# Optimization experiments

Hardware: AMD Instinct MI355X
Metric: run time of the kernel (lower is better)

Reference implementation:

```python
import jax, jax.numpy as jnp
import numpy as np

N_NODES = 100000
N_EDGES = 1600000
IN, HID, OUT = 512, 128, 64


def setup_inputs() -> dict:
    key = jax.random.key(0)
    ks = jax.random.split(key, 7)
    x = jax.random.normal(ks[0], (N_NODES, IN), dtype=jnp.float32)
    rows = jax.random.randint(ks[1], (N_EDGES,), 0, N_NODES, dtype=jnp.int32)
    cols = jax.random.randint(ks[2], (N_EDGES,), 0, N_NODES, dtype=jnp.int32)
    vals = jax.random.uniform(ks[3], (N_EDGES,), dtype=jnp.float32)
    # torch.nn.Linear weights have shape (out_features, in_features)
    W0 = jax.random.normal(ks[4], (HID, IN), dtype=jnp.float32) * (IN ** -0.5)
    W1 = jax.random.normal(ks[5], (HID, HID), dtype=jnp.float32) * (HID ** -0.5)
    W2 = jax.random.normal(ks[6], (OUT, HID), dtype=jnp.float32) * (HID ** -0.5)
    return {"x": x, "rows": rows, "cols": cols, "vals": vals,
            "W0": W0, "W1": W1, "W2": W2}


def reference(x, rows, cols, vals, W0, W1, W2):
    n = x.shape[0]

    def spmm(h):  # out[r] = sum_e vals[e] * h[cols[e]] for rows[e] == r
        return jax.ops.segment_sum(vals[:, None] * h[cols], rows, num_segments=n)

    # layer 0: Linear -> SpMM -> ReLU (dropout p=0.0 is identity)
    h = jax.nn.relu(spmm(x @ W0.T))
    # layer 1
    h = jax.nn.relu(spmm(h @ W1.T))
    # output layer: Linear -> SpMM (no activation)
    return spmm(h @ W2.T)
```

## Files before the change

kernel.cpp:

```cpp
#include <hip/hip_runtime.h>
#include <hip/hip_bf16.h>
#include <cstddef>


typedef unsigned short ushort_t;
using frag_t = __attribute__((ext_vector_type(8))) short;
using accf4 = __attribute__((ext_vector_type(4))) float;

__device__ __forceinline__ ushort_t f2bf(float f) {
    unsigned int u = __float_as_uint(f);
    u += 0x7FFF + ((u >> 16) & 1);
    return (ushort_t)(u >> 16);
}
__device__ __forceinline__ float bf2f(unsigned int u16) {
    return __uint_as_float(u16 << 16);
}


__device__ void gemm0_body(int bx, const float* __restrict__ A,
                           const float* __restrict__ W, ushort_t* __restrict__ C,
                           int M) {
    constexpr int K = 512, N = 128, BM = 128, BN = 128, BK = 64;
    constexpr int WM = BM / 2, WN = BN / 2;
    constexpr int TI = WM / 16, TJ = WN / 16;
    constexpr int LDA = BK + 8;
    constexpr int T = K / BK;
    constexpr int A_PER = BM * BK / 4 / 256;
    constexpr int B_PER = BN * BK / 4 / 256;

    __shared__ __align__(16) ushort_t As[BM][LDA];
    __shared__ __align__(16) ushort_t Bs[BN][LDA];

    const int tid = threadIdx.x;
    const int lane = tid & 63;
    const int wid = tid >> 6;
    const int wm = wid >> 1, wn = wid & 1;
    const int rowBase = bx * BM;
    const int lrow = lane & 15, kq = lane >> 4;

    float4 aF[A_PER], bF[B_PER];

    auto loadTile = [&](int k0) {
#pragma unroll
        for (int i = 0; i < A_PER; i++) {
            int idx = tid + i * 256;
            int r = idx / (BK / 4), c4 = idx % (BK / 4);
            int grow = rowBase + r;
            aF[i] = (grow < M) ? *(const float4*)(A + (size_t)grow * K + k0 + c4 * 4)
                               : make_float4(0.f, 0.f, 0.f, 0.f);
        }
#pragma unroll
        for (int i = 0; i < B_PER; i++) {
            int idx = tid + i * 256;
            int r = idx / (BK / 4), c4 = idx % (BK / 4);
            bF[i] = *(const float4*)(W + (size_t)r * K + k0 + c4 * 4);
        }
    };
    auto storeTile = [&]() {
#pragma unroll
        for (int i = 0; i < A_PER; i++) {
            int idx = tid + i * 256;
            int r = idx / (BK / 4), c4 = idx % (BK / 4);
            ushort_t p[4] = {f2bf(aF[i].x), f2bf(aF[i].y), f2bf(aF[i].z), f2bf(aF[i].w)};
            *(uint2*)&As[r][c4 * 4] = *(uint2*)p;
        }
#pragma unroll
        for (int i = 0; i < B_PER; i++) {
            int idx = tid + i * 256;
            int r = idx / (BK / 4), c4 = idx % (BK / 4);
            ushort_t p[4] = {f2bf(bF[i].x), f2bf(bF[i].y), f2bf(bF[i].z), f2bf(bF[i].w)};
            *(uint2*)&Bs[r][c4 * 4] = *(uint2*)p;
        }
    };

    accf4 acc[TI][TJ];
#pragma unroll
    for (int i = 0; i < TI; i++)
#pragma unroll
        for (int j = 0; j < TJ; j++) acc[i][j] = accf4{0.f, 0.f, 0.f, 0.f};

    loadTile(0);
    storeTile();
    __syncthreads();

    for (int t = 0; t < T; t++) {
        if (t + 1 < T) loadTile((t + 1) * BK);
#pragma unroll
        for (int ks = 0; ks < BK / 32; ks++) {
            const int kb = ks * 32 + kq * 8;
            frag_t a[TI], b[TJ];
#pragma unroll
            for (int i = 0; i < TI; i++)
                a[i] = *(const frag_t*)&As[wm * WM + i * 16 + lrow][kb];
#pragma unroll
            for (int j = 0; j < TJ; j++)
                b[j] = *(const frag_t*)&Bs[wn * WN + j * 16 + lrow][kb];
#pragma unroll
            for (int i = 0; i < TI; i++)
#pragma unroll
                for (int j = 0; j < TJ; j++)
                    acc[i][j] = __builtin_amdgcn_mfma_f32_16x16x32_bf16(
                        a[i], b[j], acc[i][j], 0, 0, 0);
        }
        __syncthreads();
        if (t + 1 < T) {
            storeTile();
            __syncthreads();
        }
    }

#pragma unroll
    for (int i = 0; i < TI; i++) {
#pragma unroll
        for (int j = 0; j < TJ; j++) {
            int col = wn * WN + j * 16 + lrow;
#pragma unroll
            for (int r = 0; r < 4; r++) {
                int grow = rowBase + wm * WM + i * 16 + kq * 4 + r;
                if (grow < M) C[(size_t)grow * N + col] = f2bf(acc[i][j][r]);
            }
        }
    }
}

__global__ __launch_bounds__(256) void d1_k(const float* __restrict__ x,
                                            const float* __restrict__ W0,
                                            ushort_t* __restrict__ g0, int M,
                                            int* __restrict__ cnt8, int m8,
                                            const float* __restrict__ W1,
                                            const float* __restrict__ W2,
                                            ushort_t* __restrict__ Wb1,
                                            ushort_t* __restrict__ Wb2,
                                            int gblocks) {
    if ((int)blockIdx.x < gblocks) {
        gemm0_body(blockIdx.x, x, W0, g0, M);
    } else {
        int i = ((int)blockIdx.x - gblocks) * 256 + threadIdx.x;
        if (i < m8) cnt8[i] = 0;
        if (i < 16384) Wb1[i] = f2bf(W1[i]);
        else if (i < 24576) Wb2[i - 16384] = f2bf(W2[i - 16384]);
    }
}


__global__ __launch_bounds__(256) void block_totals(const int* __restrict__ counts,
                                                    int* __restrict__ bsums, int n) {
    __shared__ int s[256];
    int t = threadIdx.x;
    int i = blockIdx.x * 256 + t;
    s[t] = (i < n) ? counts[i] : 0;
    __syncthreads();
    for (int off = 128; off > 0; off >>= 1) {
        if (t < off) s[t] += s[t + off];
        __syncthreads();
    }
    if (t == 0) bsums[blockIdx.x] = s[0];
}

__global__ __launch_bounds__(256) void block_totals_t(const int* __restrict__ cnt8,
                                                      int* __restrict__ bsums,
                                                      int n, int m8) {
    __shared__ int s[256];
    int t = threadIdx.x;
    int i = blockIdx.x * 256 + t;
    s[t] = (i < m8) ? cnt8[(i & 7) * n + (i >> 3)] : 0;
    __syncthreads();
    for (int off = 128; off > 0; off >>= 1) {
        if (t < off) s[t] += s[t + off];
        __syncthreads();
    }
    if (t == 0) bsums[blockIdx.x] = s[0];
}

__global__ __launch_bounds__(512) void scan_sums(int* bsums, int nb) {
    __shared__ int s[512];
    int t = threadIdx.x;
    int v = (t < nb) ? bsums[t] : 0;
    s[t] = v;
    __syncthreads();
    for (int off = 1; off < 512; off *= 2) {
        int u = (t >= off) ? s[t - off] : 0;
        __syncthreads();
        s[t] += u;
        __syncthreads();
    }
    if (t < nb) bsums[t] = s[t] - v;
}

__global__ __launch_bounds__(256) void scan_wo(const int* __restrict__ data,
                                               const int* __restrict__ offs,
                                               int* __restrict__ out0, int m) {
    __shared__ int s[256];
    int t = threadIdx.x;
    int i = blockIdx.x * 256 + t;
    int v = (i < m) ? data[i] : 0;
    s[t] = v;
    __syncthreads();
    for (int off = 1; off < 256; off *= 2) {
        int u = (t >= off) ? s[t - off] : 0;
        __syncthreads();
        s[t] += u;
        __syncthreads();
    }
    if (i < m) out0[i] = s[t] - v + offs[blockIdx.x];
}

__global__ __launch_bounds__(256) void scan_final(const int* __restrict__ cnt8,
                                                  const int* __restrict__ offs,
                                                  int* __restrict__ dstbase,
                                                  int* __restrict__ row_ptr,
                                                  int n, int ne, int m8) {
    __shared__ int s[256];
    int t = threadIdx.x;
    int i = blockIdx.x * 256 + t;
    int v = (i < m8) ? cnt8[(i & 7) * n + (i >> 3)] : 0;
    s[t] = v;
    __syncthreads();
    for (int off = 1; off < 256; off *= 2) {
        int u = (t >= off) ? s[t - off] : 0;
        __syncthreads();
        s[t] += u;
        __syncthreads();
    }
    int excl = s[t] - v + offs[blockIdx.x];
    if (i < m8) {
        dstbase[i] = excl;
        if ((i & 7) == 0) row_ptr[i >> 3] = excl;
    }
    if (i == 0) row_ptr[n] = ne;
}


__global__ __launch_bounds__(256) void hist8_k(const int* __restrict__ rows,
                                               int* __restrict__ cnt8,
                                               int* __restrict__ rank,
                                               int n, int ne) {
    int e = blockIdx.x * 256 + threadIdx.x;
    if (e >= ne) return;
    int s = blockIdx.x & 7;
    rank[e] = atomicAdd(&cnt8[s * n + rows[e]], 1);
}

__global__ __launch_bounds__(256) void scatter8_k(const int* __restrict__ rows,
                                                  const int* __restrict__ cols,
                                                  const float* __restrict__ vals,
                                                  const int* __restrict__ dstbase,
                                                  const int* __restrict__ rank,
                                                  int2* __restrict__ es, int ne) {
    int e = blockIdx.x * 256 + threadIdx.x;
    if (e >= ne) return;
    int s = blockIdx.x & 7;
    int r = rows[e];
    int p = dstbase[r * 8 + s] + rank[e];
    es[p] = make_int2(cols[e], __float_as_int(vals[e]));
}


__device__ __forceinline__ void acc8(float* acc, uint4 q, float v) {
    acc[0] += v * bf2f(q.x & 0xffff); acc[1] += v * bf2f(q.x >> 16);
    acc[2] += v * bf2f(q.y & 0xffff); acc[3] += v * bf2f(q.y >> 16);
    acc[4] += v * bf2f(q.z & 0xffff); acc[5] += v * bf2f(q.z >> 16);
    acc[6] += v * bf2f(q.w & 0xffff); acc[7] += v * bf2f(q.w >> 16);
}
__device__ __forceinline__ void acc4f(float* acc, uint2 q, float v) {
    acc[0] += v * bf2f(q.x & 0xffff); acc[1] += v * bf2f(q.x >> 16);
    acc[2] += v * bf2f(q.y & 0xffff); acc[3] += v * bf2f(q.y >> 16);
}

template <int NOUT>
__global__ __launch_bounds__(256) void spmm_mfma(const int* __restrict__ row_ptr,
                                                 const int2* __restrict__ es,
                                                 const ushort_t* __restrict__ G,
                                                 const ushort_t* __restrict__ Wb,
                                                 ushort_t* __restrict__ Hout, int n) {
    constexpr int TJ = NOUT / 64;
    constexpr int SEG = NOUT / 8;

    __shared__ __align__(16) ushort_t Hs[16][136];
    __shared__ __align__(16) ushort_t Os[16][NOUT + 8];

    const int tid = threadIdx.x;
    const int lane = tid & 63;
    const int wid = tid >> 6;
    const int g = lane >> 4, lg = lane & 15;
    const int lrow = lane & 15, kq = lane >> 4;
    const int rowBase = blockIdx.x * 16;

    frag_t bfr[4][TJ];
#pragma unroll
    for (int ks = 0; ks < 4; ks++)
#pragma unroll
        for (int j = 0; j < TJ; j++)
            bfr[ks][j] = *(const frag_t*)&Wb[(size_t)(wid * 16 * TJ + j * 16 + lrow) * 128 +
                                             ks * 32 + kq * 8];

    const ushort_t* __restrict__ Gp = G + lg * 8;
#pragma unroll
    for (int q = 0; q < 4; q++) {
        int row = rowBase + wid * 4 + q;
        float acc[8];
#pragma unroll
        for (int k = 0; k < 8; k++) acc[k] = 0.f;
        if (row < n) {
            int s = row_ptr[row];
            int e = row_ptr[row + 1];
            for (int p = s; p < e; p += 16) {
#pragma unroll
                for (int u = 0; u < 4; u++) {
                    int idx = p + u * 4 + g;
                    if (idx < e) {
                        int2 ed = es[idx];
                        uint4 qv = *(const uint4*)(Gp + (size_t)ed.x * 128);
                        acc8(acc, qv, __int_as_float(ed.y));
                    }
                }
            }
        }
#pragma unroll
        for (int k = 0; k < 8; k++) {
            acc[k] += __shfl_xor(acc[k], 16);
            acc[k] += __shfl_xor(acc[k], 32);
        }
        if (g == 0) {
            uint4 o;
            float a0 = fmaxf(acc[0], 0.f), a1 = fmaxf(acc[1], 0.f);
            float a2 = fmaxf(acc[2], 0.f), a3 = fmaxf(acc[3], 0.f);
            float a4 = fmaxf(acc[4], 0.f), a5 = fmaxf(acc[5], 0.f);
            float a6 = fmaxf(acc[6], 0.f), a7 = fmaxf(acc[7], 0.f);
            o.x = (unsigned)f2bf(a0) | ((unsigned)f2bf(a1) << 16);
            o.y = (unsigned)f2bf(a2) | ((unsigned)f2bf(a3) << 16);
            o.z = (unsigned)f2bf(a4) | ((unsigned)f2bf(a5) << 16);
            o.w = (unsigned)f2bf(a6) | ((unsigned)f2bf(a7) << 16);
            *(uint4*)&Hs[wid * 4 + q][lg * 8] = o;
        }
    }
    __syncthreads();

    accf4 oacc[TJ];
#pragma unroll
    for (int j = 0; j < TJ; j++) oacc[j] = accf4{0.f, 0.f, 0.f, 0.f};
#pragma unroll
    for (int ks = 0; ks < 4; ks++) {
        frag_t a = *(const frag_t*)&Hs[lrow][ks * 32 + kq * 8];
#pragma unroll
        for (int j = 0; j < TJ; j++)
            oacc[j] = __builtin_amdgcn_mfma_f32_16x16x32_bf16(a, bfr[ks][j], oacc[j], 0, 0, 0);
    }
#pragma unroll
    for (int j = 0; j < TJ; j++) {
        int col = wid * 16 * TJ + j * 16 + lrow;
#pragma unroll
        for (int r = 0; r < 4; r++) Os[kq * 4 + r][col] = f2bf(oacc[j][r]);
    }
    __syncthreads();

    if (tid < 16 * SEG) {
        int row16 = tid / SEG, sg = tid % SEG;
        if (rowBase + row16 < n)
            *(uint4*)&Hout[(size_t)(rowBase + row16) * NOUT + sg * 8] =
                *(const uint4*)&Os[row16][sg * 8];
    }
}


__global__ __launch_bounds__(256) void spmm_csr_64f(const int* __restrict__ row_ptr,
                                                    const int2* __restrict__ es,
                                                    const ushort_t* __restrict__ G,
                                                    float* __restrict__ H, int n) {
    int row = blockIdx.x * 4 + (threadIdx.x >> 6);
    int lane = threadIdx.x & 63;
    int g = lane >> 4, lg = lane & 15;
    if (row >= n) return;
    int s = row_ptr[row];
    int e = row_ptr[row + 1];
    float acc[4] = {0.f, 0.f, 0.f, 0.f};
    const ushort_t* __restrict__ Gp = G + lg * 4;
    for (int p = s; p < e; p += 16) {
#pragma unroll
        for (int u = 0; u < 4; u++) {
            int idx = p + u * 4 + g;
            if (idx < e) {
                int2 e0 = es[idx];
                uint2 q0 = *(const uint2*)(Gp + (size_t)e0.x * 64);
                acc4f(acc, q0, __int_as_float(e0.y));
            }
        }
    }
#pragma unroll
    for (int k = 0; k < 4; k++) {
        acc[k] += __shfl_xor(acc[k], 16);
        acc[k] += __shfl_xor(acc[k], 32);
    }
    if (g == 0) {
        float4 o = make_float4(acc[0], acc[1], acc[2], acc[3]);
        *(float4*)(H + (size_t)row * 64 + lg * 4) = o;
    }
}

static inline size_t align_up(size_t x, size_t a) { return (x + a - 1) & ~(a - 1); }

extern "C" void kernel_launch(void* const* d_in, const int* in_sizes, int n_in,
                              void* d_out, int out_size, void* d_ws, size_t ws_size,
                              hipStream_t stream) {
    const float* x = (const float*)d_in[0];
    const int* rows = (const int*)d_in[1];
    const int* cols = (const int*)d_in[2];
    const float* vals = (const float*)d_in[3];
    const float* W0 = (const float*)d_in[4];
    const float* W1 = (const float*)d_in[5];
    const float* W2 = (const float*)d_in[6];
    float* out = (float*)d_out;

    const int IN = 512, HID = 128, OUT = 64;
    const int n = in_sizes[0] / IN;
    const int ne = in_sizes[1];
    (void)OUT;

    char* ws = (char*)d_ws;
    size_t off = 0;
    ushort_t* g0 = (ushort_t*)(ws + off); off = align_up(off + (size_t)n * HID * 2, 512);
    ushort_t* g1 = (ushort_t*)(ws + off); off = align_up(off + (size_t)n * HID * 2, 512);
    ushort_t* g2 = (ushort_t*)(ws + off); off = align_up(off + (size_t)n * 64 * 2, 512);
    int2* es2 = (int2*)(ws + off); off = align_up(off + (size_t)ne * 8, 512);
    int* cnt8 = (int*)(ws + off); off = align_up(off + (size_t)8 * n * 4, 512);
    int* rank = (int*)(ws + off); off = align_up(off + (size_t)ne * 4, 512);
    int* dstbase = (int*)(ws + off); off = align_up(off + (size_t)8 * n * 4, 512);
    int* row_ptr = (int*)(ws + off); off = align_up(off + (size_t)(n + 1) * 4, 512);
    int* bsum0 = (int*)(ws + off); off = align_up(off + 4096 * 4, 512);
    int* bsum1 = (int*)(ws + off); off = align_up(off + 512 * 4, 512);
    int* off0 = (int*)(ws + off); off = align_up(off + 4096 * 4, 512);
    ushort_t* Wb1 = (ushort_t*)(ws + off); off = align_up(off + (size_t)HID * HID * 2, 512);
    ushort_t* Wb2 = (ushort_t*)(ws + off); off = align_up(off + (size_t)64 * HID * 2, 512);

    const int eb = (ne + 255) / 256;
    const int m8 = 8 * n;
    const int nb8 = (m8 + 255) / 256;
    const int nb8b = (nb8 + 255) / 256;
    const int gblocks = (n + 127) / 128;
    const int fblocks = (n + 15) / 16;
    const int sblocks = (n + 3) / 4;

    d1_k<<<gblocks + nb8, 256, 0, stream>>>(x, W0, g0, n, cnt8, m8, W1, W2,
                                            Wb1, Wb2, gblocks);

    hist8_k<<<eb, 256, 0, stream>>>(rows, cnt8, rank, n, ne);
    block_totals_t<<<nb8, 256, 0, stream>>>(cnt8, bsum0, n, m8);
    block_totals<<<nb8b, 256, 0, stream>>>(bsum0, bsum1, nb8);
    scan_sums<<<1, 512, 0, stream>>>(bsum1, nb8b);
    scan_wo<<<nb8b, 256, 0, stream>>>(bsum0, bsum1, off0, nb8);
    scan_final<<<nb8, 256, 0, stream>>>(cnt8, off0, dstbase, row_ptr, n, ne, m8);
    scatter8_k<<<eb, 256, 0, stream>>>(rows, cols, vals, dstbase, rank, es2, ne);

    spmm_mfma<128><<<fblocks, 256, 0, stream>>>(row_ptr, es2, g0, Wb1, g1, n);
    spmm_mfma<64><<<fblocks, 256, 0, stream>>>(row_ptr, es2, g1, Wb2, g2, n);
    spmm_csr_64f<<<sblocks, 256, 0, stream>>>(row_ptr, es2, g2, out, n);
}
```

Baseline: 666.7 us.

## Interleave two-row gathers in SpMM and collapse multi-level scan into one kernel

The SpMM gather loops now handle two rows per wavefront at once. Each iteration batch-loads the edges of both rows, then issues all feature-row loads before any accumulation, which raises memory-level parallelism for the random gathers. Padding edges are skipped by testing whether the value is zero. The three-kernel middle level of the prefix scan becomes a single 1024-thread kernel scanning four elements per thread, removing two launches. The pairing can waste lanes when the two rows differ in degree, and explicit edges with value 0.0 are also skipped, which is harmless because they contribute nothing.

```diff
diff --git a/kernel.cpp b/kernel.cpp
--- a/kernel.cpp
+++ b/kernel.cpp
@@ -143,20 +143,6 @@
 }
 
 
-__global__ __launch_bounds__(256) void block_totals(const int* __restrict__ counts,
-                                                    int* __restrict__ bsums, int n) {
-    __shared__ int s[256];
-    int t = threadIdx.x;
-    int i = blockIdx.x * 256 + t;
-    s[t] = (i < n) ? counts[i] : 0;
-    __syncthreads();
-    for (int off = 128; off > 0; off >>= 1) {
-        if (t < off) s[t] += s[t + off];
-        __syncthreads();
-    }
-    if (t == 0) bsums[blockIdx.x] = s[0];
-}
-
 __global__ __launch_bounds__(256) void block_totals_t(const int* __restrict__ cnt8,
                                                       int* __restrict__ bsums,
                                                       int n, int m8) {
@@ -172,37 +158,28 @@
     if (t == 0) bsums[blockIdx.x] = s[0];
 }
 
-__global__ __launch_bounds__(512) void scan_sums(int* bsums, int nb) {
-    __shared__ int s[512];
+__global__ __launch_bounds__(1024) void scan_mid(int* bsums, int nb) {
+    __shared__ int s[1024];
     int t = threadIdx.x;
-    int v = (t < nb) ? bsums[t] : 0;
-    s[t] = v;
-    __syncthreads();
-    for (int off = 1; off < 512; off *= 2) {
+    int base = t * 4;
+    int v0 = (base + 0 < nb) ? bsums[base + 0] : 0;
+    int v1 = (base + 1 < nb) ? bsums[base + 1] : 0;
+    int v2 = (base + 2 < nb) ? bsums[base + 2] : 0;
+    int v3 = (base + 3 < nb) ? bsums[base + 3] : 0;
+    int l0 = v0, l1 = l0 + v1, l2 = l1 + v2, l3 = l2 + v3;
+    s[t] = l3;
+    __syncthreads();
+    for (int off = 1; off < 1024; off *= 2) {
         int u = (t >= off) ? s[t - off] : 0;
         __syncthreads();
         s[t] += u;
         __syncthreads();
     }
-    if (t < nb) bsums[t] = s[t] - v;
-}
-
-__global__ __launch_bounds__(256) void scan_wo(const int* __restrict__ data,
-                                               const int* __restrict__ offs,
-                                               int* __restrict__ out0, int m) {
-    __shared__ int s[256];
-    int t = threadIdx.x;
-    int i = blockIdx.x * 256 + t;
-    int v = (i < m) ? data[i] : 0;
-    s[t] = v;
-    __syncthreads();
-    for (int off = 1; off < 256; off *= 2) {
-        int u = (t >= off) ? s[t - off] : 0;
-        __syncthreads();
-        s[t] += u;
-        __syncthreads();
-    }
-    if (i < m) out0[i] = s[t] - v + offs[blockIdx.x];
+    int excl = s[t] - l3;
+    if (base + 0 < nb) bsums[base + 0] = excl;
+    if (base + 1 < nb) bsums[base + 1] = excl + l0;
+    if (base + 2 < nb) bsums[base + 2] = excl + l1;
+    if (base + 3 < nb) bsums[base + 3] = excl + l2;
 }
 
 __global__ __launch_bounds__(256) void scan_final(const int* __restrict__ cnt8,
@@ -267,6 +244,46 @@
     acc[2] += v * bf2f(q.y & 0xffff); acc[3] += v * bf2f(q.y >> 16);
 }
 
+__device__ __forceinline__ void gather_pair_128(const int* __restrict__ row_ptr,
+                                                const int2* __restrict__ es,
+                                                const ushort_t* __restrict__ Gp,
+                                                int rowA, int rowB, int n,
+                                                int g, float* accA, float* accB) {
+    int sA = 0, eA = 0, sB = 0, eB = 0;
+    if (rowA < n) { sA = row_ptr[rowA]; eA = row_ptr[rowA + 1]; }
+    if (rowB < n) { sB = row_ptr[rowB]; eB = row_ptr[rowB + 1]; }
+    int nbA = (eA - sA + 15) >> 4, nbB = (eB - sB + 15) >> 4;
+    int nb = nbA > nbB ? nbA : nbB;
+    for (int b = 0; b < nb; b++) {
+        int2 edA[4], edB[4];
+#pragma unroll
+        for (int u = 0; u < 4; u++) {
+            int ia = sA + b * 16 + u * 4 + g;
+            edA[u] = (ia < eA) ? es[ia] : make_int2(0, 0);
+        }
+#pragma unroll
+        for (int u = 0; u < 4; u++) {
+            int ib = sB + b * 16 + u * 4 + g;
+            edB[u] = (ib < eB) ? es[ib] : make_int2(0, 0);
+        }
+        uint4 qA[4], qB[4];
+#pragma unroll
+        for (int u = 0; u < 4; u++) {
+            qA[u] = make_uint4(0, 0, 0, 0);
+            if (edA[u].y) qA[u] = *(const uint4*)(Gp + (size_t)edA[u].x * 128);
+        }
+#pragma unroll
+        for (int u = 0; u < 4; u++) {
+            qB[u] = make_uint4(0, 0, 0, 0);
+            if (edB[u].y) qB[u] = *(const uint4*)(Gp + (size_t)edB[u].x * 128);
+        }
+#pragma unroll
+        for (int u = 0; u < 4; u++) acc8(accA, qA[u], __int_as_float(edA[u].y));
+#pragma unroll
+        for (int u = 0; u < 4; u++) acc8(accB, qB[u], __int_as_float(edB[u].y));
+    }
+}
+
 template <int NOUT>
 __global__ __launch_bounds__(256) void spmm_mfma(const int* __restrict__ row_ptr,
                                                  const int2* __restrict__ es,
@@ -286,6 +303,40 @@
     const int lrow = lane & 15, kq = lane >> 4;
     const int rowBase = blockIdx.x * 16;
 
+    const ushort_t* __restrict__ Gp = G + lg * 8;
+#pragma unroll
+    for (int pr = 0; pr < 2; pr++) {
+        int rowA = rowBase + wid * 4 + pr * 2;
+        int rowB = rowA + 1;
+        float accA[8], accB[8];
+#pragma unroll
+        for (int k = 0; k < 8; k++) { accA[k] = 0.f; accB[k] = 0.f; }
+        gather_pair_128(row_ptr, es, Gp, rowA, rowB, n, g, accA, accB);
+#pragma unroll
+        for (int k = 0; k < 8; k++) {
+            accA[k] += __shfl_xor(accA[k], 16);
+            accA[k] += __shfl_xor(accA[k], 32);
+            accB[k] += __shfl_xor(accB[k], 16);
+            accB[k] += __shfl_xor(accB[k], 32);
+        }
+        if (g == 0) {
+            uint4 o;
+            o.x = (unsigned)f2bf(fmaxf(accA[0], 0.f)) | ((unsigned)f2bf(fmaxf(accA[1], 0.f)) << 16);
+            o.y = (unsigned)f2bf(fmaxf(accA[2], 0.f)) | ((unsigned)f2bf(fmaxf(accA[3], 0.f)) << 16);
+            o.z = (unsigned)f2bf(fmaxf(accA[4], 0.f)) | ((unsigned)f2bf(fmaxf(accA[5], 0.f)) << 16);
+            o.w = (unsigned)f2bf(fmaxf(accA[6], 0.f)) | ((unsigned)f2bf(fmaxf(accA[7], 0.f)) << 16);
+            *(uint4*)&Hs[wid * 4 + pr * 2][lg * 8] = o;
+        }
+        if (g == 1) {
+            uint4 o;
+            o.x = (unsigned)f2bf(fmaxf(accB[0], 0.f)) | ((unsigned)f2bf(fmaxf(accB[1], 0.f)) << 16);
+            o.y = (unsigned)f2bf(fmaxf(accB[2], 0.f)) | ((unsigned)f2bf(fmaxf(accB[3], 0.f)) << 16);
+            o.z = (unsigned)f2bf(fmaxf(accB[4], 0.f)) | ((unsigned)f2bf(fmaxf(accB[5], 0.f)) << 16);
+            o.w = (unsigned)f2bf(fmaxf(accB[6], 0.f)) | ((unsigned)f2bf(fmaxf(accB[7], 0.f)) << 16);
+            *(uint4*)&Hs[wid * 4 + pr * 2 + 1][lg * 8] = o;
+        }
+    }
+
     frag_t bfr[4][TJ];
 #pragma unroll
     for (int ks = 0; ks < 4; ks++)
@@ -293,47 +344,6 @@
         for (int j = 0; j < TJ; j++)
             bfr[ks][j] = *(const frag_t*)&Wb[(size_t)(wid * 16 * TJ + j * 16 + lrow) * 128 +
                                              ks * 32 + kq * 8];
-
-    const ushort_t* __restrict__ Gp = G + lg * 8;
-#pragma unroll
-    for (int q = 0; q < 4; q++) {
-        int row = rowBase + wid * 4 + q;
-        float acc[8];
-#pragma unroll
-        for (int k = 0; k < 8; k++) acc[k] = 0.f;
-        if (row < n) {
-            int s = row_ptr[row];
-            int e = row_ptr[row + 1];
-            for (int p = s; p < e; p += 16) {
-#pragma unroll
-                for (int u = 0; u < 4; u++) {
-                    int idx = p + u * 4 + g;
-                    if (idx < e) {
-                        int2 ed = es[idx];
-                        uint4 qv = *(const uint4*)(Gp + (size_t)ed.x * 128);
-                        acc8(acc, qv, __int_as_float(ed.y));
-                    }
-                }
-            }
-        }
-#pragma unroll
-        for (int k = 0; k < 8; k++) {
-            acc[k] += __shfl_xor(acc[k], 16);
-            acc[k] += __shfl_xor(acc[k], 32);
-        }
-        if (g == 0) {
-            uint4 o;
-            float a0 = fmaxf(acc[0], 0.f), a1 = fmaxf(acc[1], 0.f);
-            float a2 = fmaxf(acc[2], 0.f), a3 = fmaxf(acc[3], 0.f);
-            float a4 = fmaxf(acc[4], 0.f), a5 = fmaxf(acc[5], 0.f);
-            float a6 = fmaxf(acc[6], 0.f), a7 = fmaxf(acc[7], 0.f);
-            o.x = (unsigned)f2bf(a0) | ((unsigned)f2bf(a1) << 16);
-            o.y = (unsigned)f2bf(a2) | ((unsigned)f2bf(a3) << 16);
-            o.z = (unsigned)f2bf(a4) | ((unsigned)f2bf(a5) << 16);
-            o.w = (unsigned)f2bf(a6) | ((unsigned)f2bf(a7) << 16);
-            *(uint4*)&Hs[wid * 4 + q][lg * 8] = o;
-        }
-    }
     __syncthreads();
 
     accf4 oacc[TJ];
@@ -367,33 +377,62 @@
                                                     const int2* __restrict__ es,
                                                     const ushort_t* __restrict__ G,
                                                     float* __restrict__ H, int n) {
-    int row = blockIdx.x * 4 + (threadIdx.x >> 6);
-    int lane = threadIdx.x & 63;
-    int g = lane >> 4, lg = lane & 15;
-    if (row >= n) return;
-    int s = row_ptr[row];
-    int e = row_ptr[row + 1];
-    float acc[4] = {0.f, 0.f, 0.f, 0.f};
+    const int lane = threadIdx.x & 63;
+    const int wid = threadIdx.x >> 6;
+    const int g = lane >> 4, lg = lane & 15;
+    const int rowA = blockIdx.x * 8 + wid * 2;
+    const int rowB = rowA + 1;
+
+    int sA = 0, eA = 0, sB = 0, eB = 0;
+    if (rowA < n) { sA = row_ptr[rowA]; eA = row_ptr[rowA + 1]; }
+    if (rowB < n) { sB = row_ptr[rowB]; eB = row_ptr[rowB + 1]; }
+    int nbA = (eA - sA + 15) >> 4, nbB = (eB - sB + 15) >> 4;
+    int nb = nbA > nbB ? nbA : nbB;
+
+    float accA[4] = {0.f, 0.f, 0.f, 0.f}, accB[4] = {0.f, 0.f, 0.f, 0.f};
     const ushort_t* __restrict__ Gp = G + lg * 4;
-    for (int p = s; p < e; p += 16) {
-#pragma unroll
-        for (int u = 0; u < 4; u++) {
-            int idx = p + u * 4 + g;
-            if (idx < e) {
-                int2 e0 = es[idx];
-                uint2 q0 = *(const uint2*)(Gp + (size_t)e0.x * 64);
-                acc4f(acc, q0, __int_as_float(e0.y));
-            }
-        }
+    for (int b = 0; b < nb; b++) {
+        int2 edA[4], edB[4];
+#pragma unroll
+        for (int u = 0; u < 4; u++) {
+            int ia = sA + b * 16 + u * 4 + g;
+            edA[u] = (ia < eA) ? es[ia] : make_int2(0, 0);
+        }
+#pragma unroll
+        for (int u = 0; u < 4; u++) {
+            int ib = sB + b * 16 + u * 4 + g;
+            edB[u] = (ib < eB) ? es[ib] : make_int2(0, 0);
+        }
+        uint2 qA[4], qB[4];
+#pragma unroll
+        for (int u = 0; u < 4; u++) {
+            qA[u] = make_uint2(0, 0);
+            if (edA[u].y) qA[u] = *(const uint2*)(Gp + (size_t)edA[u].x * 64);
+        }
+#pragma unroll
+        for (int u = 0; u < 4; u++) {
+            qB[u] = make_uint2(0, 0);
+            if (edB[u].y) qB[u] = *(const uint2*)(Gp + (size_t)edB[u].x * 64);
+        }
+#pragma unroll
+        for (int u = 0; u < 4; u++) acc4f(accA, qA[u], __int_as_float(edA[u].y));
+#pragma unroll
+        for (int u = 0; u < 4; u++) acc4f(accB, qB[u], __int_as_float(edB[u].y));
     }
 #pragma unroll
     for (int k = 0; k < 4; k++) {
-        acc[k] += __shfl_xor(acc[k], 16);
-        acc[k] += __shfl_xor(acc[k], 32);
-    }
-    if (g == 0) {
-        float4 o = make_float4(acc[0], acc[1], acc[2], acc[3]);
-        *(float4*)(H + (size_t)row * 64 + lg * 4) = o;
+        accA[k] += __shfl_xor(accA[k], 16);
+        accA[k] += __shfl_xor(accA[k], 32);
+        accB[k] += __shfl_xor(accB[k], 16);
+        accB[k] += __shfl_xor(accB[k], 32);
+    }
+    if (g == 0 && rowA < n) {
+        float4 o = make_float4(accA[0], accA[1], accA[2], accA[3]);
+        *(float4*)(H + (size_t)rowA * 64 + lg * 4) = o;
+    }
+    if (g == 1 && rowB < n) {
+        float4 o = make_float4(accB[0], accB[1], accB[2], accB[3]);
+        *(float4*)(H + (size_t)rowB * 64 + lg * 4) = o;
     }
 }
 
@@ -427,31 +466,25 @@
     int* dstbase = (int*)(ws + off); off = align_up(off + (size_t)8 * n * 4, 512);
     int* row_ptr = (int*)(ws + off); off = align_up(off + (size_t)(n + 1) * 4, 512);
     int* bsum0 = (int*)(ws + off); off = align_up(off + 4096 * 4, 512);
-    int* bsum1 = (int*)(ws + off); off = align_up(off + 512 * 4, 512);
-    int* off0 = (int*)(ws + off); off = align_up(off + 4096 * 4, 512);
     ushort_t* Wb1 = (ushort_t*)(ws + off); off = align_up(off + (size_t)HID * HID * 2, 512);
     ushort_t* Wb2 = (ushort_t*)(ws + off); off = align_up(off + (size_t)64 * HID * 2, 512);
 
     const int eb = (ne + 255) / 256;
     const int m8 = 8 * n;
     const int nb8 = (m8 + 255) / 256;
-    const int nb8b = (nb8 + 255) / 256;
     const int gblocks = (n + 127) / 128;
     const int fblocks = (n + 15) / 16;
-    const int sblocks = (n + 3) / 4;
 
     d1_k<<<gblocks + nb8, 256, 0, stream>>>(x, W0, g0, n, cnt8, m8, W1, W2,
                                             Wb1, Wb2, gblocks);
 
     hist8_k<<<eb, 256, 0, stream>>>(rows, cnt8, rank, n, ne);
     block_totals_t<<<nb8, 256, 0, stream>>>(cnt8, bsum0, n, m8);
-    block_totals<<<nb8b, 256, 0, stream>>>(bsum0, bsum1, nb8);
-    scan_sums<<<1, 512, 0, stream>>>(bsum1, nb8b);
-    scan_wo<<<nb8b, 256, 0, stream>>>(bsum0, bsum1, off0, nb8);
-    scan_final<<<nb8, 256, 0, stream>>>(cnt8, off0, dstbase, row_ptr, n, ne, m8);
+    scan_mid<<<1, 1024, 0, stream>>>(bsum0, nb8);
+    scan_final<<<nb8, 256, 0, stream>>>(cnt8, bsum0, dstbase, row_ptr, n, ne, m8);
     scatter8_k<<<eb, 256, 0, stream>>>(rows, cols, vals, dstbase, rank, es2, ne);
 
     spmm_mfma<128><<<fblocks, 256, 0, stream>>>(row_ptr, es2, g0, Wb1, g1, n);
     spmm_mfma<64><<<fblocks, 256, 0, stream>>>(row_ptr, es2, g1, Wb2, g2, n);
-    spmm_csr_64f<<<sblocks, 256, 0, stream>>>(row_ptr, es2, g2, out, n);
-}
+    spmm_csr_64f<<<(n + 7) / 8, 256, 0, stream>>>(row_ptr, es2, g2, out, n);
+}
```

Result: faster. 642.1 us (-3.7%).
